# Kernel tuning notes

Hardware: AMD Instinct MI355X
Metric: run time of the kernel (lower is better)

Reference implementation:

```python
import jax, jax.numpy as jnp
import numpy as np
import math

D_MODEL = 1024
NUM_HEADS = 16
D_K = D_MODEL // NUM_HEADS
MAX_SEQ_LEN = 2048
THETA = 10000.0


def _make_rope_tables():
    inv_freq = 1.0 / (THETA ** (np.arange(0, D_K, 2, dtype=np.float32) / D_K))  # [D_K/2]
    pos = np.arange(MAX_SEQ_LEN, dtype=np.float32)
    freqs = np.einsum('i,j->ij', pos, inv_freq)                 # [S, D_K/2]
    dfreq = np.repeat(freqs, 2, axis=-1)                        # [S, D_K] (interleaved)
    return jnp.asarray(np.cos(dfreq)), jnp.asarray(np.sin(dfreq))


def setup_inputs() -> dict:
    key = jax.random.key(0)
    ks = jax.random.split(key, 5)
    std = math.sqrt(2.0 / (D_MODEL + D_MODEL))
    x = jax.random.normal(ks[0], (2, 2048, D_MODEL), dtype=jnp.float32)
    Wq = jax.random.truncated_normal(ks[1], -3.0, 3.0, (D_MODEL, D_MODEL), jnp.float32) * std
    Wk = jax.random.truncated_normal(ks[2], -3.0, 3.0, (D_MODEL, D_MODEL), jnp.float32) * std
    Wv = jax.random.truncated_normal(ks[3], -3.0, 3.0, (D_MODEL, D_MODEL), jnp.float32) * std
    Wo = jax.random.truncated_normal(ks[4], -3.0, 3.0, (D_MODEL, D_MODEL), jnp.float32) * std
    cos, sin = _make_rope_tables()
    token_positions = jnp.arange(2048, dtype=jnp.int32)
    return {"x": x, "Wq": Wq, "Wk": Wk, "Wv": Wv, "Wo": Wo,
            "cos": cos, "sin": sin, "token_positions": token_positions}


def _apply_rope(t, cos, sin, pos):
    # t: [B, H, S, D_K]; cos/sin gathered to [S, D_K], broadcast over B,H
    c = cos[pos]
    s = sin[pos]
    t1 = t[..., 0::2]
    t2 = t[..., 1::2]
    rot = jnp.stack((-t2, t1), axis=-1).reshape(t.shape)
    return t * c + rot * s


def reference(x, Wq, Wk, Wv, Wo, cos, sin, token_positions):
    B, S, _ = x.shape
    def heads(W):
        return (x @ W.T).reshape(B, S, NUM_HEADS, D_K).transpose(0, 2, 1, 3)  # [B,H,S,Dk]
    q = _apply_rope(heads(Wq), cos, sin, token_positions)
    k = _apply_rope(heads(Wk), cos, sin, token_positions)
    v = heads(Wv)
    scores = jnp.einsum('bhqd,bhkd->bhqk', q, k) / math.sqrt(D_K)
    causal = jnp.tril(jnp.ones((S, S), dtype=bool))
    scores = jnp.where(causal, scores, -jnp.inf)
    attn = jax.nn.softmax(scores, axis=-1)
    out = jnp.einsum('bhqk,bhkd->bhqd', attn, v)
    out = out.transpose(0, 2, 1, 3).reshape(B, S, D_MODEL)
    return out @ Wo.T
```

## Files before the change

kernel.cpp:

```cpp
#include <hip/hip_runtime.h>
#include <cstdint>
#include <cstddef>

#define D_MODEL 1024
#define NH 16
#define DK 64
#define S_LEN 2048

typedef __attribute__((ext_vector_type(8))) short bf16x8;
typedef __attribute__((ext_vector_type(4))) float f32x4;

#define QSCALE 0.1803368801111204f

__device__ __forceinline__ unsigned short f2bf(float f) {
    union { float f; unsigned int u; } v; v.f = f;
    unsigned int r = (v.u + 0x7fffu + ((v.u >> 16) & 1u)) >> 16;
    return (unsigned short)r;
}

#define GLL(g, l) __builtin_amdgcn_global_load_lds( \
    (const __attribute__((address_space(1))) unsigned int*)(g), \
    (__attribute__((address_space(3))) unsigned int*)(l), 16, 0, 0)

__global__ __launch_bounds__(256) void convert_bf16(
    const float* __restrict__ x,
    const float* __restrict__ wq, const float* __restrict__ wk,
    const float* __restrict__ wv, const float* __restrict__ wo,
    unsigned short* __restrict__ Xb, unsigned short* __restrict__ Wb,
    unsigned short* __restrict__ Wob)
{
    const unsigned t = blockIdx.x * 256 + threadIdx.x;
    const float* src;
    unsigned short* dst;
    if (t < 1048576u)      { src = x  + 4 * (size_t)t;               dst = Xb  + 4 * (size_t)t; }
    else if (t < 1310720u) { size_t i = t - 1048576u; src = wq + 4*i; dst = Wb + 4*i; }
    else if (t < 1572864u) { size_t i = t - 1310720u; src = wk + 4*i; dst = Wb + 1048576u + 4*i; }
    else if (t < 1835008u) { size_t i = t - 1572864u; src = wv + 4*i; dst = Wb + 2097152u + 4*i; }
    else                   { size_t i = t - 1835008u; src = wo + 4*i; dst = Wob + 4*i; }
    float4 v = *(const float4*)src;
    unsigned short pk[4] = {f2bf(v.x), f2bf(v.y), f2bf(v.z), f2bf(v.w)};
    *(uint2*)dst = *(const uint2*)pk;
}


#define CP 132
__global__ __launch_bounds__(256) void gemm_qkv(
    const unsigned short* __restrict__ Xb, const unsigned short* __restrict__ Wb,
    const float* __restrict__ cosT, const float* __restrict__ sinT,
    const int* __restrict__ posArr,
    unsigned short* __restrict__ Qo, unsigned short* __restrict__ Ko,
    unsigned short* __restrict__ Vt)
{
    __shared__ __align__(16) unsigned short smem[128 * CP];
    unsigned short* As = smem;
    unsigned short* Bs = smem + 128 * 64;
    unsigned short* Cs = smem;

    const int tid  = threadIdx.x;
    const int wave = tid >> 6;
    const int lane = tid & 63;
    const int m16  = lane & 15;
    const int quad = lane >> 4;
    const int warpM = (wave >> 1) * 64;
    const int warpN = (wave & 1) * 64;
    const int rowBase = blockIdx.y * 128;
    const int colBase = blockIdx.x * 128;

    const int l8  = lane >> 3;
    const int lb  = lane & 7;
    const int cbl = (lb ^ l8) * 8;

    f32x4 acc[4][4];
#pragma unroll
    for (int i = 0; i < 4; ++i)
#pragma unroll
        for (int j = 0; j < 4; ++j) acc[i][j] = (f32x4){0.f, 0.f, 0.f, 0.f};

    for (int k0 = 0; k0 < D_MODEL; k0 += 64) {
        __syncthreads();
#pragma unroll
        for (int it = 0; it < 4; ++it) {
            const int r = wave * 32 + it * 8 + l8;
            const int dstOff = wave * 2048 + it * 512 + lane * 8;
            GLL(Xb + (size_t)(rowBase + r) * D_MODEL + k0 + cbl, &As[dstOff]);
            GLL(Wb + (size_t)(colBase + r) * D_MODEL + k0 + cbl, &Bs[dstOff]);
        }
        __asm__ volatile("s_waitcnt vmcnt(0)" ::: "memory");
        __syncthreads();
#pragma unroll
        for (int ks = 0; ks < 2; ++ks) {
            bf16x8 af[4], bf[4];
#pragma unroll
            for (int t4 = 0; t4 < 4; ++t4) {
                const int rowA = warpM + t4 * 16 + m16;
                const int rowB = warpN + t4 * 16 + m16;
                const int cb = ((ks * 4 + quad) ^ (m16 & 7)) * 8;
                af[t4] = *(const bf16x8*)&As[rowA * 64 + cb];
                bf[t4] = *(const bf16x8*)&Bs[rowB * 64 + cb];
            }
#pragma unroll
            for (int mt = 0; mt < 4; ++mt)
#pragma unroll
                for (int nt = 0; nt < 4; ++nt)
                    acc[mt][nt] = __builtin_amdgcn_mfma_f32_16x16x32_bf16(
                        af[mt], bf[nt], acc[mt][nt], 0, 0, 0);
        }
    }

    const int which = (colBase + warpN) >> 10;
    if (which == 2) {
#pragma unroll
        for (int mt = 0; mt < 4; ++mt) {
            const int gr0 = rowBase + warpM + mt * 16 + quad * 4;
            const int b   = gr0 >> 11;
            const int s0  = gr0 & 2047;
#pragma unroll
            for (int nt = 0; nt < 4; ++nt) {
                const int c1 = (colBase + warpN + nt * 16 + m16) & 1023;
                const int h  = c1 >> 6;
                const int d  = c1 & 63;
                unsigned short pk[4];
#pragma unroll
                for (int r = 0; r < 4; ++r) pk[r] = f2bf(acc[mt][nt][r]);
                *(uint2*)(Vt + ((size_t)(b * NH + h) * DK + d) * S_LEN + s0) =
                    *(const uint2*)pk;
            }
        }
    } else {
        __syncthreads();
#pragma unroll
        for (int mt = 0; mt < 4; ++mt) {
            const int lr0 = warpM + mt * 16 + quad * 4;
#pragma unroll
            for (int nt = 0; nt < 4; ++nt) {
                const int lc = warpN + nt * 16 + m16;
                const int d  = lc & 63;
#pragma unroll
                for (int r = 0; r < 4; ++r) {
                    const int s = (rowBase + lr0 + r) & 2047;
                    const int p = posArr[s];
                    float v = acc[mt][nt][r];
                    float o = __shfl_xor(v, 1, 64);
                    float c  = cosT[(size_t)p * DK + d];
                    float sn = sinT[(size_t)p * DK + d];
                    float res = (d & 1) ? (v * c + o * sn) : (v * c - o * sn);
                    if (which == 0) res *= QSCALE;
                    Cs[(lr0 + r) * CP + lc] = f2bf(res);
                }
            }
        }
        __syncthreads();
        unsigned short* outB = (which == 0) ? Qo : Ko;
        const int r2   = tid >> 1;
        const int half = tid & 1;
        const int gr   = rowBase + r2;
        const int b    = gr >> 11;
        const int s    = gr & 2047;
        const int h    = ((colBase & 1023) + half * 64) >> 6;
        unsigned short* dst = outB + ((size_t)(b * NH + h) * S_LEN + s) * DK;
        const unsigned short* srcp = &Cs[r2 * CP + half * 64];
#pragma unroll
        for (int j = 0; j < 8; ++j)
            ((uint4*)dst)[j] = ((const uint4*)srcp)[j];
    }
}

__global__ __launch_bounds__(256) void gemm_proj(
    const unsigned short* __restrict__ A, const unsigned short* __restrict__ B,
    float* __restrict__ C)
{
    __shared__ __align__(16) unsigned short As[128 * 64];
    __shared__ __align__(16) unsigned short Bs[128 * 64];

    const int tid  = threadIdx.x;
    const int wave = tid >> 6;
    const int lane = tid & 63;
    const int m16  = lane & 15;
    const int quad = lane >> 4;
    const int warpM = (wave >> 1) * 64;
    const int warpN = (wave & 1) * 64;
    const int rowBase = blockIdx.y * 128;
    const int colBase = blockIdx.x * 128;

    const int l8  = lane >> 3;
    const int lb  = lane & 7;
    const int cbl = (lb ^ l8) * 8;

    f32x4 acc[4][4];
#pragma unroll
    for (int i = 0; i < 4; ++i)
#pragma unroll
        for (int j = 0; j < 4; ++j) acc[i][j] = (f32x4){0.f, 0.f, 0.f, 0.f};

    for (int k0 = 0; k0 < D_MODEL; k0 += 64) {
        __syncthreads();
#pragma unroll
        for (int it = 0; it < 4; ++it) {
            const int r = wave * 32 + it * 8 + l8;
            const int dstOff = wave * 2048 + it * 512 + lane * 8;
            GLL(A + (size_t)(rowBase + r) * D_MODEL + k0 + cbl, &As[dstOff]);
            GLL(B + (size_t)(colBase + r) * D_MODEL + k0 + cbl, &Bs[dstOff]);
        }
        __asm__ volatile("s_waitcnt vmcnt(0)" ::: "memory");
        __syncthreads();
#pragma unroll
        for (int ks = 0; ks < 2; ++ks) {
            bf16x8 af[4], bf[4];
#pragma unroll
            for (int t4 = 0; t4 < 4; ++t4) {
                const int rowA = warpM + t4 * 16 + m16;
                const int rowB = warpN + t4 * 16 + m16;
                const int cb = ((ks * 4 + quad) ^ (m16 & 7)) * 8;
                af[t4] = *(const bf16x8*)&As[rowA * 64 + cb];
                bf[t4] = *(const bf16x8*)&Bs[rowB * 64 + cb];
            }
#pragma unroll
            for (int mt = 0; mt < 4; ++mt)
#pragma unroll
                for (int nt = 0; nt < 4; ++nt)
                    acc[mt][nt] = __builtin_amdgcn_mfma_f32_16x16x32_bf16(
                        af[mt], bf[nt], acc[mt][nt], 0, 0, 0);
        }
    }

#pragma unroll
    for (int mt = 0; mt < 4; ++mt)
#pragma unroll
        for (int reg = 0; reg < 4; ++reg) {
            int gr = rowBase + warpM + mt * 16 + quad * 4 + reg;
            float* crow = C + (size_t)gr * D_MODEL + colBase + warpN;
#pragma unroll
            for (int nt = 0; nt < 4; ++nt)
                crow[nt * 16 + m16] = acc[mt][nt][reg];
        }
}

__global__ __launch_bounds__(256, 3) void flash_mfma(
    const unsigned short* __restrict__ Q,
    const unsigned short* __restrict__ K,
    const unsigned short* __restrict__ Vt,
    unsigned short* __restrict__ O)
{
    const int g    = blockIdx.x;
    const int qt   = 31 - (g >> 5);
    const int bh   = g & 31;
    const int b    = bh >> 4;
    const int h    = bh & 15;
    const int tid  = threadIdx.x;
    const int wave = tid >> 6;
    const int lane = tid & 63;
    const int m16  = lane & 15;
    const int quad = lane >> 4;
    const int l8   = lane >> 3;
    const int nIter = (qt >> 1) + 1;

    __shared__ __align__(16) unsigned short Ks[128 * 64];
    __shared__ __align__(16) unsigned short VsT[64 * 128];
    __shared__ __align__(16) unsigned short Ps[64][136];

    const unsigned short* Qg = Q + ((size_t)bh * S_LEN + qt * 64) * DK;
#pragma unroll
    for (int it = 0; it < 2; ++it) {
        const int rb = wave * 16 + it * 8;
        const int r  = rb + l8;
        const int cb = ((lane & 7) ^ (r & 7)) * 8;
        GLL(Qg + r * DK + cb, &Ks[rb * 64 + lane * 8]);
    }
    __asm__ volatile("s_waitcnt vmcnt(0)" ::: "memory");
    __syncthreads();
    const int qrow = wave * 16 + m16;
    const bf16x8 qf0 = *(const bf16x8*)&Ks[qrow * 64 + ((quad ^ (m16 & 7)) * 8)];
    const bf16x8 qf1 = *(const bf16x8*)&Ks[qrow * 64 + (((4 + quad) ^ (m16 & 7)) * 8)];

    const short one_bf = (short)0x3F80;
    const bf16x8 ones8 = {one_bf, one_bf, one_bf, one_bf,
                          one_bf, one_bf, one_bf, one_bf};

    f32x4 o[4];
    f32x4 lacc = (f32x4){0.f, 0.f, 0.f, 0.f};
#pragma unroll
    for (int r = 0; r < 4; ++r) o[r] = (f32x4){0.f, 0.f, 0.f, 0.f};

    const unsigned short* Kg0 = K + (size_t)bh * S_LEN * DK;
    const unsigned short* Vg0 = Vt + (size_t)bh * DK * S_LEN;

    for (int kb = 0; kb < nIter; ++kb) {
        const int ko = kb * 128;
        __syncthreads();
#pragma unroll
        for (int it = 0; it < 4; ++it) {
            const int rb = wave * 32 + it * 8;
            const int r  = rb + l8;
            const int cb = ((lane & 7) ^ (r & 7)) * 8;
            GLL(Kg0 + (size_t)(ko + r) * DK + cb, &Ks[rb * 64 + lane * 8]);
        }
#pragma unroll
        for (int it = 0; it < 4; ++it) {
            const int db = wave * 16 + it * 4;
            const int d  = db + (lane >> 4);
            const int cb = ((lane & 15) ^ (d & 15)) * 8;
            GLL(Vg0 + (size_t)d * S_LEN + ko + cb, &VsT[db * 128 + lane * 8]);
        }
        __asm__ volatile("s_waitcnt vmcnt(0)" ::: "memory");
        __syncthreads();

        f32x4 s[8];
#pragma unroll
        for (int ct = 0; ct < 8; ++ct) {
            const int kr = ct * 16 + m16;
            bf16x8 kf0 = *(const bf16x8*)&Ks[kr * 64 + ((quad ^ (m16 & 7)) * 8)];
            bf16x8 kf1 = *(const bf16x8*)&Ks[kr * 64 + (((4 + quad) ^ (m16 & 7)) * 8)];
            f32x4 z = {0.f, 0.f, 0.f, 0.f};
            z = __builtin_amdgcn_mfma_f32_16x16x32_bf16(qf0, kf0, z, 0, 0, 0);
            z = __builtin_amdgcn_mfma_f32_16x16x32_bf16(qf1, kf1, z, 0, 0, 0);
            s[ct] = z;
        }

        if (kb == nIter - 1) {
#pragma unroll
            for (int ct = 0; ct < 8; ++ct)
#pragma unroll
                for (int r = 0; r < 4; ++r) {
                    int colk = ko + ct * 16 + m16;
                    int row  = qt * 64 + wave * 16 + quad * 4 + r;
                    if (colk > row) s[ct][r] = -16384.f;
                }
        }

#pragma unroll
        for (int ct = 0; ct < 8; ++ct)
#pragma unroll
            for (int r = 0; r < 4; ++r)
                Ps[wave * 16 + quad * 4 + r][ct * 16 + m16] =
                    f2bf(__builtin_exp2f(s[ct][r]));

        __asm__ volatile("s_waitcnt lgkmcnt(0)" ::: "memory");

        bf16x8 pf[4];
#pragma unroll
        for (int kc = 0; kc < 4; ++kc)
            pf[kc] = *(const bf16x8*)&Ps[wave * 16 + m16][kc * 32 + quad * 8];
#pragma unroll
        for (int kc = 0; kc < 4; ++kc)
            lacc = __builtin_amdgcn_mfma_f32_16x16x32_bf16(pf[kc], ones8, lacc, 0, 0, 0);
#pragma unroll
        for (int ct = 0; ct < 4; ++ct) {
            const int vr = ct * 16 + m16;
#pragma unroll
            for (int kc = 0; kc < 4; ++kc) {
                bf16x8 vf = *(const bf16x8*)
                    &VsT[vr * 128 + (((kc * 4 + quad) ^ m16) * 8)];
                o[ct] = __builtin_amdgcn_mfma_f32_16x16x32_bf16(pf[kc], vf, o[ct], 0, 0, 0);
            }
        }
    }

    float inv[4];
#pragma unroll
    for (int r = 0; r < 4; ++r) inv[r] = 1.0f / lacc[r];
#pragma unroll
    for (int r = 0; r < 4; ++r) {
        int srow = qt * 64 + wave * 16 + quad * 4 + r;
        unsigned short* orow = O + (((size_t)b * S_LEN + srow) * NH + h) * DK;
#pragma unroll
        for (int ct = 0; ct < 4; ++ct)
            orow[ct * 16 + m16] = f2bf(o[ct][r] * inv[r]);
    }
}

extern "C" void kernel_launch(void* const* d_in, const int* in_sizes, int n_in,
                              void* d_out, int out_size, void* d_ws, size_t ws_size,
                              hipStream_t stream)
{
    const float* x      = (const float*)d_in[0];
    const float* Wq     = (const float*)d_in[1];
    const float* Wk     = (const float*)d_in[2];
    const float* Wv     = (const float*)d_in[3];
    const float* Wo     = (const float*)d_in[4];
    const float* cosT   = (const float*)d_in[5];
    const float* sinT   = (const float*)d_in[6];
    const int*   posArr = (const int*)d_in[7];
    float* out = (float*)d_out;

    unsigned short* ws0 = (unsigned short*)d_ws;
    unsigned short* Xb  = ws0;
    unsigned short* Wb  = ws0 + 4194304;
    unsigned short* Wob = ws0 + 7340032;
    unsigned short* Qw  = ws0 + 8388608;
    unsigned short* Kw  = ws0 + 12582912;
    unsigned short* Vtw = ws0 + 16777216;
    unsigned short* Ow  = ws0 + 20971520;

    convert_bf16<<<8192, 256, 0, stream>>>(x, Wq, Wk, Wv, Wo, Xb, Wb, Wob);

    gemm_qkv<<<dim3(3072 / 128, 4096 / 128), 256, 0, stream>>>(
        Xb, Wb, cosT, sinT, posArr, Qw, Kw, Vtw);

    flash_mfma<<<1024, 256, 0, stream>>>(Qw, Kw, Vtw, Ow);

    gemm_proj<<<dim3(D_MODEL / 128, 4096 / 128), 256, 0, stream>>>(Ow, Wob, out);
}
```

Measured before the change: 225.2 us.

## Double-buffer LDS tiles in QKV and output-projection GEMMs

Both the QKV GEMM and the output projection GEMM now keep two LDS buffers for their A/B tiles. The global-to-LDS loads for the next K step are issued before computing on the current buffer, and a partial vmcnt wait lets those loads overlap the MFMA work. Shared memory per block doubles to 64 KB, which may lower occupancy. A second barrier per iteration now guards buffer reuse.

Result: faster. 201.5 us (-10.5%).

```diff
diff --git a/kernel.cpp b/kernel.cpp
--- a/kernel.cpp
+++ b/kernel.cpp
@@ -51,9 +51,7 @@
     unsigned short* __restrict__ Qo, unsigned short* __restrict__ Ko,
     unsigned short* __restrict__ Vt)
 {
-    __shared__ __align__(16) unsigned short smem[128 * CP];
-    unsigned short* As = smem;
-    unsigned short* Bs = smem + 128 * 64;
+    __shared__ __align__(16) unsigned short smem[4 * 128 * 64];
     unsigned short* Cs = smem;
 
     const int tid  = threadIdx.x;
@@ -70,23 +68,39 @@
     const int lb  = lane & 7;
     const int cbl = (lb ^ l8) * 8;
 
+    const unsigned short* Arow = Xb + (size_t)rowBase * D_MODEL;
+    const unsigned short* Brow = Wb + (size_t)colBase * D_MODEL;
+
     f32x4 acc[4][4];
 #pragma unroll
     for (int i = 0; i < 4; ++i)
 #pragma unroll
         for (int j = 0; j < 4; ++j) acc[i][j] = (f32x4){0.f, 0.f, 0.f, 0.f};
 
-    for (int k0 = 0; k0 < D_MODEL; k0 += 64) {
-        __syncthreads();
+    auto stage = [&](int k0, int bsel) {
+        unsigned short* As = smem + bsel * 16384;
+        unsigned short* Bs = As + 8192;
 #pragma unroll
         for (int it = 0; it < 4; ++it) {
             const int r = wave * 32 + it * 8 + l8;
             const int dstOff = wave * 2048 + it * 512 + lane * 8;
-            GLL(Xb + (size_t)(rowBase + r) * D_MODEL + k0 + cbl, &As[dstOff]);
-            GLL(Wb + (size_t)(colBase + r) * D_MODEL + k0 + cbl, &Bs[dstOff]);
-        }
-        __asm__ volatile("s_waitcnt vmcnt(0)" ::: "memory");
-        __syncthreads();
+            GLL(Arow + (size_t)r * D_MODEL + k0 + cbl, &As[dstOff]);
+            GLL(Brow + (size_t)r * D_MODEL + k0 + cbl, &Bs[dstOff]);
+        }
+    };
+
+    stage(0, 0);
+    for (int it = 0; it < 16; ++it) {
+        const int cur = it & 1;
+        if (it < 15) {
+            stage((it + 1) * 64, cur ^ 1);
+            __asm__ volatile("s_waitcnt vmcnt(8)" ::: "memory");
+        } else {
+            __asm__ volatile("s_waitcnt vmcnt(0)" ::: "memory");
+        }
+        __syncthreads();
+        const unsigned short* As = smem + cur * 16384;
+        const unsigned short* Bs = As + 8192;
 #pragma unroll
         for (int ks = 0; ks < 2; ++ks) {
             bf16x8 af[4], bf[4];
@@ -105,6 +119,7 @@
                     acc[mt][nt] = __builtin_amdgcn_mfma_f32_16x16x32_bf16(
                         af[mt], bf[nt], acc[mt][nt], 0, 0, 0);
         }
+        __syncthreads();
     }
 
     const int which = (colBase + warpN) >> 10;
@@ -127,7 +142,6 @@
             }
         }
     } else {
-        __syncthreads();
 #pragma unroll
         for (int mt = 0; mt < 4; ++mt) {
             const int lr0 = warpM + mt * 16 + quad * 4;
@@ -169,8 +183,7 @@
     const unsigned short* __restrict__ A, const unsigned short* __restrict__ B,
     float* __restrict__ C)
 {
-    __shared__ __align__(16) unsigned short As[128 * 64];
-    __shared__ __align__(16) unsigned short Bs[128 * 64];
+    __shared__ __align__(16) unsigned short smem[4 * 128 * 64];
 
     const int tid  = threadIdx.x;
     const int wave = tid >> 6;
@@ -186,23 +199,39 @@
     const int lb  = lane & 7;
     const int cbl = (lb ^ l8) * 8;
 
+    const unsigned short* Arow = A + (size_t)rowBase * D_MODEL;
+    const unsigned short* Brow = B + (size_t)colBase * D_MODEL;
+
     f32x4 acc[4][4];
 #pragma unroll
     for (int i = 0; i < 4; ++i)
 #pragma unroll
         for (int j = 0; j < 4; ++j) acc[i][j] = (f32x4){0.f, 0.f, 0.f, 0.f};
 
-    for (int k0 = 0; k0 < D_MODEL; k0 += 64) {
-        __syncthreads();
+    auto stage = [&](int k0, int bsel) {
+        unsigned short* As = smem + bsel * 16384;
+        unsigned short* Bs = As + 8192;
 #pragma unroll
         for (int it = 0; it < 4; ++it) {
             const int r = wave * 32 + it * 8 + l8;
             const int dstOff = wave * 2048 + it * 512 + lane * 8;
-            GLL(A + (size_t)(rowBase + r) * D_MODEL + k0 + cbl, &As[dstOff]);
-            GLL(B + (size_t)(colBase + r) * D_MODEL + k0 + cbl, &Bs[dstOff]);
-        }
-        __asm__ volatile("s_waitcnt vmcnt(0)" ::: "memory");
-        __syncthreads();
+            GLL(Arow + (size_t)r * D_MODEL + k0 + cbl, &As[dstOff]);
+            GLL(Brow + (size_t)r * D_MODEL + k0 + cbl, &Bs[dstOff]);
+        }
+    };
+
+    stage(0, 0);
+    for (int it = 0; it < 16; ++it) {
+        const int cur = it & 1;
+        if (it < 15) {
+            stage((it + 1) * 64, cur ^ 1);
+            __asm__ volatile("s_waitcnt vmcnt(8)" ::: "memory");
+        } else {
+            __asm__ volatile("s_waitcnt vmcnt(0)" ::: "memory");
+        }
+        __syncthreads();
+        const unsigned short* As = smem + cur * 16384;
+        const unsigned short* Bs = As + 8192;
 #pragma unroll
         for (int ks = 0; ks < 2; ++ks) {
             bf16x8 af[4], bf[4];
@@ -221,6 +250,7 @@
                     acc[mt][nt] = __builtin_amdgcn_mfma_f32_16x16x32_bf16(
                         af[mt], bf[nt], acc[mt][nt], 0, 0, 0);
         }
+        __syncthreads();
     }
 
 #pragma unroll
```
